# Performance work log

Hardware: AMD Instinct MI355X
Metric: run time of the kernel (lower is better)

Reference implementation:

```python
import jax, jax.numpy as jnp
import numpy as np
import math

B, S, DIM = 2, 2048, 2048
NH = 16
HD = DIM // NH  # 128
RANK = 32


def setup_inputs() -> dict:
    key = jax.random.key(0)
    ks = jax.random.split(key, 10)
    x = jax.random.normal(ks[0], (B, S, DIM), dtype=jnp.float32)
    # causal additive mask (use -1e9 instead of -inf for grad-safety)
    mask = jnp.where(jnp.tril(jnp.ones((S, S), dtype=bool)), 0.0, -1e9).astype(jnp.float32)[None, None]
    # rotary frequencies, as in llama: theta = 10000^{-2i/d}
    inv_freq = 1.0 / (10000.0 ** (jnp.arange(0, HD, 2, dtype=jnp.float32) / HD))  # [HD/2]
    t = jnp.arange(S, dtype=jnp.float32)
    freqs = jnp.outer(t, inv_freq)  # [S, HD/2]
    freqs_cos = jnp.cos(freqs)
    freqs_sin = jnp.sin(freqs)
    scale = 0.02
    wq = jax.random.normal(ks[1], (DIM, DIM), dtype=jnp.float32) * scale
    wk = jax.random.normal(ks[2], (DIM, DIM), dtype=jnp.float32) * scale
    wv = jax.random.normal(ks[3], (DIM, DIM), dtype=jnp.float32) * scale
    wo = jax.random.normal(ks[4], (DIM, DIM), dtype=jnp.float32) * scale
    wa_q = jax.random.normal(ks[5], (RANK, DIM), dtype=jnp.float32) * 0.02
    wa_k = jax.random.normal(ks[6], (RANK, DIM), dtype=jnp.float32) * 0.02
    return {"x": x, "mask": mask, "freqs_cos": freqs_cos, "freqs_sin": freqs_sin,
            "wq": wq, "wk": wk, "wv": wv, "wo": wo, "wa_q": wa_q, "wa_k": wa_k}


def _apply_rope(t, cos, sin):
    # t: [B, S, H, HD]; cos/sin: [S, HD/2]
    tr = t.reshape(*t.shape[:-1], HD // 2, 2)
    tre, tim = tr[..., 0], tr[..., 1]
    c = cos[None, :, None, :]
    s = sin[None, :, None, :]
    out_re = tre * c - tim * s
    out_im = tre * s + tim * c
    return jnp.stack([out_re, out_im], axis=-1).reshape(t.shape)


def reference(x, mask, freqs_cos, freqs_sin, wq, wk, wv, wo, wa_q, wa_k):
    bsz, seqlen, dim = x.shape
    xq = (x @ wq.T).reshape(bsz, seqlen, NH, HD)
    xk = (x @ wk.T).reshape(bsz, seqlen, NH, HD)
    xv = (x @ wv.T).reshape(bsz, seqlen, NH, HD)
    # low-rank adaptive gate (computed on detached x in the original)
    xd = jax.lax.stop_gradient(x)
    xq_h = xd @ wa_q.T  # [B, S, 32]
    xk_h = xd @ wa_k.T  # [B, S, 32]
    adaptive_mask = jnp.einsum('bqr,bkr->bqk', xq_h, xk_h)  # [B, S, S]

    xq = _apply_rope(xq, freqs_cos, freqs_sin)
    xk = _apply_rope(xk, freqs_cos, freqs_sin)

    q = xq.transpose(0, 2, 1, 3)  # [B, H, S, HD]
    k = xk.transpose(0, 2, 1, 3)
    v = xv.transpose(0, 2, 1, 3)

    scores = jnp.einsum('bhqd,bhkd->bhqk', q, k) / math.sqrt(HD)
    scores = scores + mask
    scores = jax.nn.softmax(scores.astype(jnp.float32), axis=-1).astype(q.dtype)
    scores = scores * jax.nn.sigmoid(adaptive_mask)[:, None]  # gate, broadcast over heads
    out = jnp.einsum('bhqk,bhkd->bhqd', scores, v)
    out = out.transpose(0, 2, 1, 3).reshape(bsz, seqlen, -1)
    return out @ wo.T
```

## Files before the change

### kernel.cpp

```cpp
#include <hip/hip_runtime.h>

typedef __attribute__((ext_vector_type(8))) short short8v;
typedef __attribute__((ext_vector_type(4))) short short4v;
typedef __attribute__((ext_vector_type(4))) float floatx4;
typedef __attribute__((ext_vector_type(2))) int int2v;

#define S_    2048
#define DIM_  2048
#define NW_   6400
#define VOFF_ 4352

#define ASG(p) ((__attribute__((address_space(1))) void*)(p))
#define ASL(p) ((__attribute__((address_space(3))) void*)(p))

__device__ __forceinline__ short f2bf(float f){
  union { float f; unsigned u; } c; c.f = f;
  unsigned u = c.u;
  unsigned r = (u + 0x7fffu + ((u >> 16) & 1u)) >> 16;
  return (short)r;
}
__device__ __forceinline__ float bf2f(short s){
  union { unsigned u; float f; } c; c.u = ((unsigned)(unsigned short)s) << 16;
  return c.f;
}

__global__ __launch_bounds__(256) void cvt_k(const float* __restrict__ in,
                                             short* __restrict__ out, int n){
  int i = blockIdx.x*256 + threadIdx.x;
  int idx = i*4;
  if (idx >= n) return;
  floatx4 v = *(const floatx4*)(in + idx);
  short4v o;
  o[0]=f2bf(v[0]); o[1]=f2bf(v[1]); o[2]=f2bf(v[2]); o[3]=f2bf(v[3]);
  *(short4v*)(out + idx) = o;
}

__global__ __launch_bounds__(256)
void cvt_w(const float* wq, const float* waq, const float* wak,
           const float* wk, const float* wv, const float* wo,
           short* Wcat, short* wob){
  const float* src; short* dst; int n;
  int bx = blockIdx.x;
  switch (blockIdx.y){
    case 0: src=wq; dst=Wcat;                   n=4194304; break;
    case 1: src=wk; dst=Wcat+(size_t)2112*2048; n=4194304; break;
    case 2: src=wv; dst=Wcat+(size_t)4352*2048; n=4194304; break;
    case 3: src=wo; dst=wob;                    n=4194304; break;
    default:
      if (bx < 64)      { src=waq; dst=Wcat+(size_t)2048*2048; n=65536; }
      else if (bx < 128){ src=wak; dst=Wcat+(size_t)2080*2048; n=65536; bx-=64; }
      else if (bx < 512){
        int idx = ((bx-128)*256 + threadIdx.x)*4;
        if (idx < 393216){
          short4v z = {0,0,0,0};
          *(short4v*)(Wcat + (size_t)4160*2048 + idx) = z;
        }
        return;
      } else return;
  }
  int idx = (bx*256 + threadIdx.x)*4;
  if (idx >= n) return;
  floatx4 v = *(const floatx4*)(src + idx);
  short4v o;
  o[0]=f2bf(v[0]); o[1]=f2bf(v[1]); o[2]=f2bf(v[2]); o[3]=f2bf(v[3]);
  *(short4v*)(dst + idx) = o;
}

__global__ __launch_bounds__(512,2)
void gemm_qkv(const short* __restrict__ A, const short* __restrict__ B,
              short* __restrict__ Cout, short* __restrict__ Vt, int bofs){
  __shared__ short SH[65536];
  const int K = 2048;
  int tid = threadIdx.x;
  int wave = tid>>6, lane = tid&63, quad = lane>>4, l16 = lane&15;
  int wm_i = wave>>2, wn_i = wave&3;

  int bid = blockIdx.x + bofs;
  int swz = (bid&7)*50 + (bid>>3);
  int m0 = (swz & 15)*256;
  int n0 = (swz >> 4)*256;

  int srow = tid>>2;
  int sseg = (tid&3) ^ ((srow ^ (srow>>2)) & 3);
  const short* aS = A + (size_t)(m0 + srow)*K + sseg*8;
  const short* bS = B + (size_t)(n0 + srow)*K + sseg*8;
  int sdst = wave*512;

  int sx   = (l16 ^ (l16>>2)) & 3;
  int aoff = (wm_i*128 + l16)*32 + (quad^sx)*8;
  int boff = (wn_i*64  + l16)*32 + (quad^sx)*8;

  floatx4 acc[8][4] = {};
  short8v afA[8], afB[8], bfA[4], bfB[4];

#define QSTAGE(src, chunk) do{ \
    __builtin_amdgcn_global_load_lds(ASG(src), ASL(&SH[(chunk)+sdst]), 16, 0, 0); \
    __builtin_amdgcn_global_load_lds(ASG((src) + (size_t)128*2048), ASL(&SH[(chunk)+sdst+4096]), 16, 0, 0); \
  }while(0)
#define QBAR  asm volatile("s_barrier" ::: "memory")
#define QW4   asm volatile("s_waitcnt vmcnt(4)" ::: "memory")
#define MFMA_ __builtin_amdgcn_mfma_f32_16x16x32_bf16

  QSTAGE(aS,            0);
  QSTAGE(bS,        32768);
  QSTAGE(aS+32,      8192);
  QSTAGE(bS+32, 32768+8192);
  QW4;
  QBAR;
  #pragma unroll
  for (int mf=0; mf<4; ++mf) afA[mf] = *(short8v*)&SH[0     + mf*512 + aoff];
  #pragma unroll
  for (int nf=0; nf<4; ++nf) bfA[nf] = *(short8v*)&SH[32768 + nf*512 + boff];
  QSTAGE(aS + 64, 16384);

  for (int t=0; t<32; ++t){
    int buf = t&1, nb = buf^1;
    int A0c = buf*16384,        A1c = A0c+8192;
    int B0c = 32768+buf*16384,  B1c = B0c+8192;
    int A0n = nb*16384,         A1n = A0n+8192;
    int B0n = 32768+nb*16384,   B1n = B0n+8192;
    int kn  = ((t+1)&31)*64;
    int kn2 = ((t+2)&31)*64;

    #pragma unroll
    for (int mf=4; mf<8; ++mf) afA[mf] = *(short8v*)&SH[A0c + mf*512 + aoff];
    QSTAGE(bS + kn, B0n);
    QW4;
    QBAR;
    __builtin_amdgcn_s_setprio(1);
    #pragma unroll
    for (int mf=0; mf<4; ++mf)
      #pragma unroll
      for (int nf=0; nf<4; ++nf)
        acc[mf][nf] = MFMA_(afA[mf], bfA[nf], acc[mf][nf], 0,0,0);
    __builtin_amdgcn_s_setprio(0);

    #pragma unroll
    for (int mf=0; mf<4; ++mf) afB[mf] = *(short8v*)&SH[A1c + mf*512 + aoff];
    #pragma unroll
    for (int nf=0; nf<4; ++nf) bfB[nf] = *(short8v*)&SH[B1c + nf*512 + boff];
    QSTAGE(aS + kn + 32, A1n);
    QBAR;
    __builtin_amdgcn_s_setprio(1);
    #pragma unroll
    for (int mf=4; mf<8; ++mf)
      #pragma unroll
      for (int nf=0; nf<4; ++nf)
        acc[mf][nf] = MFMA_(afA[mf], bfA[nf], acc[mf][nf], 0,0,0);
    __builtin_amdgcn_s_setprio(0);

    #pragma unroll
    for (int mf=4; mf<8; ++mf) afB[mf] = *(short8v*)&SH[A1c + mf*512 + aoff];
    QSTAGE(bS + kn + 32, B1n);
    QW4;
    QBAR;
    __builtin_amdgcn_s_setprio(1);
    #pragma unroll
    for (int mf=0; mf<4; ++mf)
      #pragma unroll
      for (int nf=0; nf<4; ++nf)
        acc[mf][nf] = MFMA_(afB[mf], bfB[nf], acc[mf][nf], 0,0,0);
    __builtin_amdgcn_s_setprio(0);

    #pragma unroll
    for (int mf=0; mf<4; ++mf) afA[mf] = *(short8v*)&SH[A0n + mf*512 + aoff];
    #pragma unroll
    for (int nf=0; nf<4; ++nf) bfA[nf] = *(short8v*)&SH[B0n + nf*512 + boff];
    QSTAGE(aS + kn2, A0c);
    QBAR;
    __builtin_amdgcn_s_setprio(1);
    #pragma unroll
    for (int mf=4; mf<8; ++mf)
      #pragma unroll
      for (int nf=0; nf<4; ++nf)
        acc[mf][nf] = MFMA_(afB[mf], bfB[nf], acc[mf][nf], 0,0,0);
    __builtin_amdgcn_s_setprio(0);
  }

  __syncthreads();

  if (n0 < VOFF_){
    #pragma unroll
    for (int mf=0; mf<8; ++mf)
      #pragma unroll
      for (int r=0; r<4; ++r){
        size_t gm = (size_t)(m0 + wm_i*128 + mf*16 + quad*4 + r);
        #pragma unroll
        for (int nf=0; nf<4; ++nf)
          Cout[gm*NW_ + n0 + wn_i*64 + nf*16 + l16] = f2bf(acc[mf][nf][r]);
      }
  } else {
    short* T = SH;
    #pragma unroll
    for (int mf=0; mf<8; ++mf){
      int mb = wm_i*128 + mf*16 + quad*4;
      int mc = mb>>3, mi = mb&7;
      #pragma unroll
      for (int nf=0; nf<4; ++nf){
        int n = wn_i*64 + nf*16 + l16;
        short4v p;
        p[0]=f2bf(acc[mf][nf][0]); p[1]=f2bf(acc[mf][nf][1]);
        p[2]=f2bf(acc[mf][nf][2]); p[3]=f2bf(acc[mf][nf][3]);
        *(short4v*)&T[n*256 + ((mc ^ (n&31))*8) + mi] = p;
      }
    }
    __syncthreads();
    int f = tid>>1, half = tid&1;
    size_t vbase = (size_t)(n0 - VOFF_ + f)*4096 + m0;
    #pragma unroll
    for (int c=0; c<16; ++c){
      int cc = half*16 + c;
      short8v v = *(short8v*)&T[f*256 + ((cc ^ (f&31))*8)];
      *(short8v*)&Vt[vbase + cc*8] = v;
    }
  }
#undef QSTAGE
#undef QBAR
#undef QW4
#undef MFMA_
}

__global__ __launch_bounds__(256,4)
void gemm_nt_f32(const short* __restrict__ A, const short* __restrict__ B,
                 float* __restrict__ Cout, int M, int N, int K){
  __shared__ short As[128][64];
  __shared__ short Bs[128][64];
  int tid = threadIdx.x;
  int wave = tid>>6, lane = tid&63, quad = lane>>4, l16 = lane&15;
  int l7 = l16&7;
  int m0 = blockIdx.x*128, n0 = blockIdx.y*128;
  int wm = (wave>>1)*64, wn = (wave&1)*64;
  floatx4 acc[4][4] = {};

  int lr = lane>>3;
  int sw = (lane&7) ^ lr;
  const short* Abase = A + (size_t)(m0 + wave*32 + lr)*K + sw*8;
  const short* Bbase = B + (size_t)(n0 + wave*32 + lr)*K + sw*8;

  for (int k0 = 0; k0 < K; k0 += 64){
    __syncthreads();
    #pragma unroll
    for (int i=0;i<4;i++){
      __builtin_amdgcn_global_load_lds(ASG(Abase + (size_t)(i*8)*K + k0),
                                       ASL(&As[wave*32 + i*8][0]), 16, 0, 0);
      __builtin_amdgcn_global_load_lds(ASG(Bbase + (size_t)(i*8)*K + k0),
                                       ASL(&Bs[wave*32 + i*8][0]), 16, 0, 0);
    }
    __syncthreads();
    #pragma unroll
    for (int ks=0; ks<2; ks++){
      short8v af[4], bf[4];
      #pragma unroll
      for (int i=0;i<4;i++) af[i] = *(short8v*)&As[wm + i*16 + l16][((ks*4+quad)^l7)*8];
      #pragma unroll
      for (int j=0;j<4;j++) bf[j] = *(short8v*)&Bs[wn + j*16 + l16][((ks*4+quad)^l7)*8];
      #pragma unroll
      for (int i=0;i<4;i++)
        #pragma unroll
        for (int j=0;j<4;j++)
          acc[i][j] = __builtin_amdgcn_mfma_f32_16x16x32_bf16(af[i], bf[j], acc[i][j], 0,0,0);
    }
  }
  #pragma unroll
  for (int i=0;i<4;i++)
    #pragma unroll
    for (int r=0;r<4;r++){
      int gm = m0 + wm + i*16 + quad*4 + r;
      #pragma unroll
      for (int j=0;j<4;j++){
        int gn = n0 + wn + j*16 + l16;
        Cout[(size_t)gm*N + gn] = acc[i][j][r];
      }
    }
}

__global__ __launch_bounds__(256) void rope_k(short* __restrict__ X,
                                              const float* __restrict__ fcos,
                                              const float* __restrict__ fsin){
  int i = blockIdx.x*256 + threadIdx.x;
  int row = i >> 9;
  int p0  = (i & 511)*2;
  int s = row & (S_-1);
  int pp = p0 & 63;
  float c0 = fcos[s*64+pp],   sn0 = fsin[s*64+pp];
  float c1 = fcos[s*64+pp+1], sn1 = fsin[s*64+pp+1];
  size_t a = (size_t)row*NW_ + 2112 + p0*2;
  int2v v = *(int2v*)(X + a);
  float re0 = bf2f((short)(v[0] & 0xffff)), im0 = bf2f((short)(v[0] >> 16));
  float re1 = bf2f((short)(v[1] & 0xffff)), im1 = bf2f((short)(v[1] >> 16));
  int2v o;
  o[0] = ((int)(unsigned short)f2bf(re0*sn0 + im0*c0) << 16) | (unsigned short)f2bf(re0*c0 - im0*sn0);
  o[1] = ((int)(unsigned short)f2bf(re1*sn1 + im1*c1) << 16) | (unsigned short)f2bf(re1*c1 - im1*sn1);
  *(int2v*)(X + a) = o;
}

__global__ __launch_bounds__(256)
void gate_k(const short* __restrict__ X, short* __restrict__ G){
  int kt = blockIdx.x, qt = blockIdx.y, b = blockIdx.z;
  if (kt > qt) return;
  int tid = threadIdx.x, wave = tid>>6, lane = tid&63, quad = lane>>4, l16 = lane&15;
  const float NL2E = -1.44269504f;

  short8v qh = *(const short8v*)&X[(size_t)(b*2048 + qt*64 + wave*16 + l16)*NW_ + 2048 + quad*8];
  floatx4 am[4];
  #pragma unroll
  for (int j=0;j<4;j++){
    short8v kh = *(const short8v*)&X[(size_t)(b*2048 + kt*64 + j*16 + l16)*NW_ + 2080 + quad*8];
    floatx4 z = {0.f,0.f,0.f,0.f};
    am[j] = __builtin_amdgcn_mfma_f32_16x16x32_bf16(qh, kh, z, 0,0,0);
  }
  short* Gd = G + (((size_t)(b*32 + kt)*2048) + qt*64 + wave*16 + quad*4)*64 + l16*4;
  #pragma unroll
  for (int r=0;r<4;r++){
    short4v sv;
    #pragma unroll
    for (int j=0;j<4;j++){
      float g = __builtin_amdgcn_rcpf(1.f + __builtin_amdgcn_exp2f(am[j][r]*NL2E));
      sv[j] = f2bf(g);
    }
    *(short4v*)(Gd + (size_t)r*64) = sv;
  }
}

__global__ __launch_bounds__(256,2)
void flash_k(const short* __restrict__ Qc, const short* __restrict__ Vt,
             const short* __restrict__ G, const float* __restrict__ fcos,
             const float* __restrict__ fsin, short* __restrict__ O){
  int h = blockIdx.x, pi = blockIdx.y, b = blockIdx.z;
  int tid = threadIdx.x, wave = tid>>6, lane = tid&63, quad = lane>>4, l16 = lane&15;
  int l7 = l16&7;

  __shared__ short Ks [64][128];
  __shared__ short Vts[128][64];
  __shared__ short Ps [4][16][72];

  const float CS = 1.44269504f * 0.08838834764831845f;

  for (int ph = 0; ph < 2; ph++){
    int qt = ph ? pi : 31 - pi;
    int srow = qt*64 + wave*16 + l16;
    size_t qrow = (size_t)(b*2048 + srow);
    short8v qf[4];
    #pragma unroll
    for (int ks=0;ks<4;ks++)
      qf[ks] = *(const short8v*)&Qc[qrow*NW_ + h*128 + ks*32 + quad*8];
    #pragma unroll
    for (int ks=0;ks<4;ks++)
      #pragma unroll
      for (int jj=0;jj<4;jj++){
        float re = bf2f(qf[ks][2*jj]), im = bf2f(qf[ks][2*jj+1]);
        int p = ks*16 + quad*4 + jj;
        float c = fcos[srow*64 + p], sn = fsin[srow*64 + p];
        qf[ks][2*jj]   = f2bf(re*c - im*sn);
        qf[ks][2*jj+1] = f2bf(re*sn + im*c);
      }

    floatx4 oacc[8] = {};
    float lp[4] = {0.f,0.f,0.f,0.f};

    for (int kt=0; kt<=qt; kt++){
      int k0 = kt*64;
      __syncthreads();
      {
        const short* Ksrc = Qc + ((size_t)(b*2048 + k0 + wave*16))*NW_ + 2112 + h*128;
        int r4 = lane>>4, c16 = lane&15;
        #pragma unroll
        for (int j=0;j<4;j++)
          __builtin_amdgcn_global_load_lds(
            ASG(Ksrc + (size_t)(j*4 + r4)*NW_ + ((c16 ^ r4 ^ ((j&1)*4))*8)),
            ASL(&Ks[wave*16 + j*4][0]), 16, 0, 0);
        const short* Vsrc = Vt + ((size_t)(h*128 + wave*32 + (lane>>3)))*4096 + b*2048 + k0
                            + (((lane&7) ^ (lane>>3))*8);
        #pragma unroll
        for (int j=0;j<4;j++)
          __builtin_amdgcn_global_load_lds(
            ASG(Vsrc + (size_t)(j*8)*4096),
            ASL(&Vts[wave*32 + j*8][0]), 16, 0, 0);
      }
      __syncthreads();

      const short* gb = G + (((size_t)(b*32 + kt)*2048) + qt*64 + wave*16 + quad*4)*64 + l16*4;
      short4v g4[4];
      #pragma unroll
      for (int r=0;r<4;r++) g4[r] = *(const short4v*)(gb + (size_t)r*64);

      floatx4 sacc[4] = {};
      #pragma unroll
      for (int j=0;j<4;j++)
        #pragma unroll
        for (int ks2=0;ks2<4;ks2++){
          short8v kf = *(short8v*)&Ks[j*16+l16][((ks2*4+quad)^l7)*8];
          sacc[j] = __builtin_amdgcn_mfma_f32_16x16x32_bf16(qf[ks2], kf, sacc[j], 0,0,0);
        }

      bool diag = (kt == qt);
      int qbase = wave*16 + quad*4;
      #pragma unroll
      for (int j=0;j<4;j++){
        int kin = j*16 + l16;
        #pragma unroll
        for (int r=0;r<4;r++){
          bool keep = !diag || (kin <= qbase + r);
          float p = keep ? __builtin_amdgcn_exp2f(sacc[j][r]*CS) : 0.f;
          lp[r] += p;
          Ps[wave][quad*4+r][j*16+l16] = f2bf(p * bf2f(g4[r][j]));
        }
      }

      #pragma unroll
      for (int ks2=0; ks2<2; ks2++){
        short8v pf = *(short8v*)&Ps[wave][l16][ks2*32 + quad*8];
        #pragma unroll
        for (int dt=0; dt<8; dt++){
          short8v vf = *(short8v*)&Vts[dt*16 + l16][((ks2*4+quad)^l7)*8];
          oacc[dt] = __builtin_amdgcn_mfma_f32_16x16x32_bf16(pf, vf, oacc[dt], 0,0,0);
        }
      }
    }

    #pragma unroll
    for (int r=0;r<4;r++)
      #pragma unroll
      for (int off=1; off<16; off<<=1)
        lp[r] += __shfl_xor(lp[r], off, 64);
    #pragma unroll
    for (int r=0;r<4;r++){
      float inv = __builtin_amdgcn_rcpf(lp[r]);
      size_t orow = (size_t)(b*2048 + qt*64 + wave*16 + quad*4 + r);
      #pragma unroll
      for (int dt=0;dt<8;dt++)
        O[orow*2048 + h*128 + dt*16 + l16] = f2bf(oacc[dt][r]*inv);
    }
  }
}

extern "C" void kernel_launch(void* const* d_in, const int* in_sizes, int n_in,
                              void* d_out, int out_size, void* d_ws, size_t ws_size,
                              hipStream_t stream){
  const float* x    = (const float*)d_in[0];
  const float* fcos = (const float*)d_in[2];
  const float* fsin = (const float*)d_in[3];
  const float* wq   = (const float*)d_in[4];
  const float* wk   = (const float*)d_in[5];
  const float* wv   = (const float*)d_in[6];
  const float* wo   = (const float*)d_in[7];
  const float* waq  = (const float*)d_in[8];
  const float* wak  = (const float*)d_in[9];
  float* out = (float*)d_out;

  char* ws = (char*)d_ws;
  size_t off = 0;
  short* xb   = (short*)(ws + off); off += (size_t)4096*2048*2;
  short* Wcat = (short*)(ws + off); off += (size_t)NW_*2048*2;
  short* wob  = (short*)(ws + off); off += (size_t)2048*2048*2;
  short* XQKV = (short*)(ws + off); off += (size_t)4096*NW_*2;
  short* Vtb  = (short*)(ws + off); off += (size_t)2048*4096*2;
  short* G    = xb;
  short* Ob   = Wcat;

  cvt_k<<<8192,256,0,stream>>>(x, xb, 8388608);
  cvt_w<<<dim3(4096,5),256,0,stream>>>(wq, waq, wak, wk, wv, wo, Wcat, wob);

  gemm_qkv<<<dim3(256),512,0,stream>>>(xb, Wcat, XQKV, Vtb, 0);
  gemm_qkv<<<dim3(144),512,0,stream>>>(xb, Wcat, XQKV, Vtb, 256);

  rope_k<<<8192,256,0,stream>>>(XQKV, fcos, fsin);
  gate_k<<<dim3(32,32,2),256,0,stream>>>(XQKV, G);

  flash_k<<<dim3(16,16,2),256,0,stream>>>(XQKV, Vtb, G, fcos, fsin, Ob);

  gemm_nt_f32<<<dim3(32,16),256,0,stream>>>(Ob, wob, out, 4096, 2048, 2048);
}
```

Measured before the change: 413.2 us.

## Merge conversion, QKV GEMM, and rope/gate launches; pack bf16 P stores

The x and weight conversion kernels become one launch, the two QKV GEMM launches become a single 400-block launch, and the rope and gate kernels become one kernel that branches on block id. In the flash kernel, probability values are gathered per row and converted with the packed v_cvt_pk_bf16_f32 instruction instead of per-element software rounding. The goal is fewer kernel launches and gaps between them, plus fewer ALU instructions in the softmax path. The merged rope_gate kernel mixes two unrelated workloads in one grid, and gate blocks read the rope region without ordering; this looks safe only because the gate reads the low-rank columns, which rope does not touch.

```diff
diff --git a/kernel.cpp b/kernel.cpp
--- a/kernel.cpp
+++ b/kernel.cpp
@@ -24,39 +24,27 @@
   return c.f;
 }
 
-__global__ __launch_bounds__(256) void cvt_k(const float* __restrict__ in,
-                                             short* __restrict__ out, int n){
-  int i = blockIdx.x*256 + threadIdx.x;
-  int idx = i*4;
-  if (idx >= n) return;
-  floatx4 v = *(const floatx4*)(in + idx);
-  short4v o;
-  o[0]=f2bf(v[0]); o[1]=f2bf(v[1]); o[2]=f2bf(v[2]); o[3]=f2bf(v[3]);
-  *(short4v*)(out + idx) = o;
-}
-
 __global__ __launch_bounds__(256)
-void cvt_w(const float* wq, const float* waq, const float* wak,
-           const float* wk, const float* wv, const float* wo,
-           short* Wcat, short* wob){
-  const float* src; short* dst; int n;
-  int bx = blockIdx.x;
-  switch (blockIdx.y){
-    case 0: src=wq; dst=Wcat;                   n=4194304; break;
-    case 1: src=wk; dst=Wcat+(size_t)2112*2048; n=4194304; break;
-    case 2: src=wv; dst=Wcat+(size_t)4352*2048; n=4194304; break;
-    case 3: src=wo; dst=wob;                    n=4194304; break;
-    default:
-      if (bx < 64)      { src=waq; dst=Wcat+(size_t)2048*2048; n=65536; }
-      else if (bx < 128){ src=wak; dst=Wcat+(size_t)2080*2048; n=65536; bx-=64; }
-      else if (bx < 512){
-        int idx = ((bx-128)*256 + threadIdx.x)*4;
-        if (idx < 393216){
-          short4v z = {0,0,0,0};
-          *(short4v*)(Wcat + (size_t)4160*2048 + idx) = z;
-        }
-        return;
-      } else return;
+void cvt_all(const float* __restrict__ x,  const float* __restrict__ wq,
+             const float* __restrict__ wk, const float* __restrict__ wv,
+             const float* __restrict__ wo, const float* __restrict__ waq,
+             const float* __restrict__ wak,
+             short* __restrict__ xb, short* __restrict__ Wcat,
+             short* __restrict__ wob){
+  int bid = blockIdx.x;
+  const float* src; short* dst; int n, bx;
+  if      (bid <  8192){ src=x;   dst=xb;                         n=8388608; bx=bid; }
+  else if (bid < 12288){ src=wq;  dst=Wcat;                       n=4194304; bx=bid-8192; }
+  else if (bid < 16384){ src=wk;  dst=Wcat+(size_t)2112*2048;     n=4194304; bx=bid-12288; }
+  else if (bid < 20480){ src=wv;  dst=Wcat+(size_t)4352*2048;     n=4194304; bx=bid-16384; }
+  else if (bid < 24576){ src=wo;  dst=wob;                        n=4194304; bx=bid-20480; }
+  else if (bid < 24640){ src=waq; dst=Wcat+(size_t)2048*2048;     n=65536;   bx=bid-24576; }
+  else if (bid < 24704){ src=wak; dst=Wcat+(size_t)2080*2048;     n=65536;   bx=bid-24640; }
+  else {
+    int idx = ((bid-24704)*256 + threadIdx.x)*4;
+    short4v z = {0,0,0,0};
+    *(short4v*)(Wcat + (size_t)4160*2048 + idx) = z;
+    return;
   }
   int idx = (bx*256 + threadIdx.x)*4;
   if (idx >= n) return;
@@ -68,14 +56,14 @@
 
 __global__ __launch_bounds__(512,2)
 void gemm_qkv(const short* __restrict__ A, const short* __restrict__ B,
-              short* __restrict__ Cout, short* __restrict__ Vt, int bofs){
+              short* __restrict__ Cout, short* __restrict__ Vt){
   __shared__ short SH[65536];
   const int K = 2048;
   int tid = threadIdx.x;
   int wave = tid>>6, lane = tid&63, quad = lane>>4, l16 = lane&15;
   int wm_i = wave>>2, wn_i = wave&3;
 
-  int bid = blockIdx.x + bofs;
+  int bid = blockIdx.x;
   int swz = (bid&7)*50 + (bid>>3);
   int m0 = (swz & 15)*256;
   int n0 = (swz >> 4)*256;
@@ -274,29 +262,30 @@
     }
 }
 
-__global__ __launch_bounds__(256) void rope_k(short* __restrict__ X,
-                                              const float* __restrict__ fcos,
-                                              const float* __restrict__ fsin){
-  int i = blockIdx.x*256 + threadIdx.x;
-  int row = i >> 9;
-  int p0  = (i & 511)*2;
-  int s = row & (S_-1);
-  int pp = p0 & 63;
-  float c0 = fcos[s*64+pp],   sn0 = fsin[s*64+pp];
-  float c1 = fcos[s*64+pp+1], sn1 = fsin[s*64+pp+1];
-  size_t a = (size_t)row*NW_ + 2112 + p0*2;
-  int2v v = *(int2v*)(X + a);
-  float re0 = bf2f((short)(v[0] & 0xffff)), im0 = bf2f((short)(v[0] >> 16));
-  float re1 = bf2f((short)(v[1] & 0xffff)), im1 = bf2f((short)(v[1] >> 16));
-  int2v o;
-  o[0] = ((int)(unsigned short)f2bf(re0*sn0 + im0*c0) << 16) | (unsigned short)f2bf(re0*c0 - im0*sn0);
-  o[1] = ((int)(unsigned short)f2bf(re1*sn1 + im1*c1) << 16) | (unsigned short)f2bf(re1*c1 - im1*sn1);
-  *(int2v*)(X + a) = o;
-}
-
 __global__ __launch_bounds__(256)
-void gate_k(const short* __restrict__ X, short* __restrict__ G){
-  int kt = blockIdx.x, qt = blockIdx.y, b = blockIdx.z;
+void rope_gate(short* __restrict__ X, const float* __restrict__ fcos,
+               const float* __restrict__ fsin, short* __restrict__ G){
+  int bid = blockIdx.x;
+  if (bid < 8192){
+    int i = bid*256 + threadIdx.x;
+    int row = i >> 9;
+    int p0  = (i & 511)*2;
+    int s = row & (S_-1);
+    int pp = p0 & 63;
+    float c0 = fcos[s*64+pp],   sn0 = fsin[s*64+pp];
+    float c1 = fcos[s*64+pp+1], sn1 = fsin[s*64+pp+1];
+    size_t a = (size_t)row*NW_ + 2112 + p0*2;
+    int2v v = *(int2v*)(X + a);
+    float re0 = bf2f((short)(v[0] & 0xffff)), im0 = bf2f((short)(v[0] >> 16));
+    float re1 = bf2f((short)(v[1] & 0xffff)), im1 = bf2f((short)(v[1] >> 16));
+    int2v o;
+    o[0] = ((int)(unsigned short)f2bf(re0*sn0 + im0*c0) << 16) | (unsigned short)f2bf(re0*c0 - im0*sn0);
+    o[1] = ((int)(unsigned short)f2bf(re1*sn1 + im1*c1) << 16) | (unsigned short)f2bf(re1*c1 - im1*sn1);
+    *(int2v*)(X + a) = o;
+    return;
+  }
+  int g = bid - 8192;
+  int kt = g & 31, qt = (g>>5)&31, b = g>>10;
   if (kt > qt) return;
   int tid = threadIdx.x, wave = tid>>6, lane = tid&63, quad = lane>>4, l16 = lane&15;
   const float NL2E = -1.44269504f;
@@ -315,8 +304,8 @@
     short4v sv;
     #pragma unroll
     for (int j=0;j<4;j++){
-      float g = __builtin_amdgcn_rcpf(1.f + __builtin_amdgcn_exp2f(am[j][r]*NL2E));
-      sv[j] = f2bf(g);
+      float gg = __builtin_amdgcn_rcpf(1.f + __builtin_amdgcn_exp2f(am[j][r]*NL2E));
+      sv[j] = f2bf(gg);
     }
     *(short4v*)(Gd + (size_t)r*64) = sv;
   }
@@ -395,16 +384,29 @@
 
       bool diag = (kt == qt);
       int qbase = wave*16 + quad*4;
-      #pragma unroll
-      for (int j=0;j<4;j++){
-        int kin = j*16 + l16;
-        #pragma unroll
-        for (int r=0;r<4;r++){
+      float pv0[4], pv1[4], pv2[4], pv3[4];
+      #pragma unroll
+      for (int r=0;r<4;r++){
+        #pragma unroll
+        for (int j=0;j<4;j++){
+          int kin = j*16 + l16;
           bool keep = !diag || (kin <= qbase + r);
           float p = keep ? __builtin_amdgcn_exp2f(sacc[j][r]*CS) : 0.f;
           lp[r] += p;
-          Ps[wave][quad*4+r][j*16+l16] = f2bf(p * bf2f(g4[r][j]));
+          float g = p * bf2f(g4[r][j]);
+          if (j==0) pv0[r]=g; else if (j==1) pv1[r]=g; else if (j==2) pv2[r]=g; else pv3[r]=g;
         }
+      }
+      #pragma unroll
+      for (int r=0;r<4;r++){
+        unsigned u01, u23;
+        asm("v_cvt_pk_bf16_f32 %0, %1, %2" : "=v"(u01) : "v"(pv0[r]), "v"(pv1[r]));
+        asm("v_cvt_pk_bf16_f32 %0, %1, %2" : "=v"(u23) : "v"(pv2[r]), "v"(pv3[r]));
+        short* Prow = &Ps[wave][quad*4+r][l16];
+        Prow[ 0] = (short)(u01 & 0xffffu);
+        Prow[16] = (short)(u01 >> 16);
+        Prow[32] = (short)(u23 & 0xffffu);
+        Prow[48] = (short)(u23 >> 16);
       }
 
       #pragma unroll
@@ -458,14 +460,11 @@
   short* G    = xb;
   short* Ob   = Wcat;
 
-  cvt_k<<<8192,256,0,stream>>>(x, xb, 8388608);
-  cvt_w<<<dim3(4096,5),256,0,stream>>>(wq, waq, wak, wk, wv, wo, Wcat, wob);
-
-  gemm_qkv<<<dim3(256),512,0,stream>>>(xb, Wcat, XQKV, Vtb, 0);
-  gemm_qkv<<<dim3(144),512,0,stream>>>(xb, Wcat, XQKV, Vtb, 256);
-
-  rope_k<<<8192,256,0,stream>>>(XQKV, fcos, fsin);
-  gate_k<<<dim3(32,32,2),256,0,stream>>>(XQKV, G);
+  cvt_all<<<25088,256,0,stream>>>(x, wq, wk, wv, wo, waq, wak, xb, Wcat, wob);
+
+  gemm_qkv<<<dim3(400),512,0,stream>>>(xb, Wcat, XQKV, Vtb);
+
+  rope_gate<<<10240,256,0,stream>>>(XQKV, fcos, fsin, G);
 
   flash_k<<<dim3(16,16,2),256,0,stream>>>(XQKV, Vtb, G, fcos, fsin, Ob);
 
```

After: 412.8 us. About the same (-0.1%).
